# Kernel optimization log

Hardware: AMD Instinct MI355X
Metric: run time of the kernel (lower is better)

Reference implementation:

```python
import jax, jax.numpy as jnp
import numpy as np

G = 7  # grid size hardcoded in the original loops


def _xyxy(t, off, m, n):
    # t: (B, C, G, G); channels off..off+3 are (x_off, y_off, w, h)
    cx = (t[:, off + 0] + m) / G
    cy = (t[:, off + 1] + n) / G
    w = t[:, off + 2]
    h = t[:, off + 3]
    return cx - w / 2, cy - h / 2, cx + w / 2, cy + h / 2


def _iou(a, b):
    ix1 = jnp.maximum(a[0], b[0])
    iy1 = jnp.maximum(a[1], b[1])
    ix2 = jnp.minimum(a[2], b[2])
    iy2 = jnp.minimum(a[3], b[3])
    inter = jnp.maximum(ix2 - ix1, 0.0) * jnp.maximum(iy2 - iy1, 0.0)
    area_a = (a[2] - a[0]) * (a[3] - a[1])
    area_b = (b[2] - b[0]) * (b[3] - b[1])
    return jnp.where(inter > 0, inter / (area_a + area_b - inter), 0.0)


def setup_inputs() -> dict:
    key = jax.random.key(0)
    k1, k2, k3 = jax.random.split(key, 3)
    B = 8192
    pred = jax.random.uniform(k1, (B, 30, G, G), dtype=jnp.float32)
    labels = jax.random.uniform(k2, (B, 30, G, G), dtype=jnp.float32)
    # objectness channel must be exactly 1.0 for cells containing objects
    obj = (jax.random.uniform(k3, (B, G, G)) < 0.3).astype(jnp.float32)
    labels = labels.at[:, 4].set(obj)
    return {"pred": pred, "labels": labels}


def reference(pred, labels):
    B = pred.shape[0]
    dt = pred.dtype
    m = jnp.arange(G, dtype=dt)[:, None]  # index along dim -2 (as in loop var m)
    n = jnp.arange(G, dtype=dt)[None, :]  # index along dim -1 (loop var n)

    b1 = _xyxy(pred, 0, m, n)
    b2 = _xyxy(pred, 5, m, n)
    gt = _xyxy(labels, 0, m, n)
    iou1 = _iou(b1, gt)  # (B, G, G)
    iou2 = _iou(b2, gt)
    use1 = iou1 >= iou2
    obj = labels[:, 4] == 1.0

    coor1 = (jnp.sum((pred[:, 0:2] - labels[:, 0:2]) ** 2, axis=1)
             + jnp.sum((jnp.sqrt(pred[:, 2:4]) - jnp.sqrt(labels[:, 2:4])) ** 2, axis=1))
    coor2 = (jnp.sum((pred[:, 5:7] - labels[:, 5:7]) ** 2, axis=1)
             + jnp.sum((jnp.sqrt(pred[:, 7:9]) - jnp.sqrt(labels[:, 7:9])) ** 2, axis=1))
    coor = 5.0 * jnp.where(use1, coor1, coor2)

    e1 = (pred[:, 4] - iou1) ** 2
    e2 = (pred[:, 9] - iou2) ** 2
    obj_conf = jnp.where(use1, e1, e2)
    noobj_conf_objcell = 0.5 * jnp.where(use1, e2, e1)
    noobj_conf_nocell = 0.5 * (pred[:, 4] ** 2 + pred[:, 9] ** 2)

    cls = jnp.sum((pred[:, 10:] - labels[:, 10:]) ** 2, axis=1)

    per_cell = jnp.where(obj,
                         coor + obj_conf + noobj_conf_objcell + cls,
                         noobj_conf_nocell)
    return jnp.sum(per_cell) / B
```

## Files before the change

kernel.cpp:

```cpp
#include <hip/hip_runtime.h>

#define GDIM 7
#define CELLS 49
#define CH 30
#define FPB (CH * CELLS)
#define BLK 256

__device__ __forceinline__ float iou_fn(float ax1, float ay1, float ax2, float ay2,
                                        float bx1, float by1, float bx2, float by2) {
    float ix1 = fmaxf(ax1, bx1);
    float iy1 = fmaxf(ay1, by1);
    float ix2 = fminf(ax2, bx2);
    float iy2 = fminf(ay2, by2);
    float iw = fmaxf(ix2 - ix1, 0.0f);
    float ih = fmaxf(iy2 - iy1, 0.0f);
    float inter = iw * ih;
    float aa = (ax2 - ax1) * (ay2 - ay1);
    float ab = (bx2 - bx1) * (by2 - by1);
    return inter > 0.0f ? inter / (aa + ab - inter) : 0.0f;
}

__global__ __launch_bounds__(BLK) void yolo_stage1(const float* __restrict__ pred,
                                                   const float* __restrict__ lab,
                                                   float* __restrict__ partial) {
    const int tid = threadIdx.x;
    const int i = blockIdx.x * BLK + tid;

    const int b = i / CELLS;
    const int cell = i - b * CELLS;
    const int mr = cell / GDIM;
    const int nc = cell - mr * GDIM;
    const float* p = pred + (size_t)b * FPB + cell;
    const float* l = lab  + (size_t)b * FPB + cell;

    float pv[10], lv[10];
    #pragma unroll
    for (int c = 0; c < 10; ++c) pv[c] = p[c * CELLS];
    #pragma unroll
    for (int c = 0; c < 10; ++c) lv[c] = l[c * CELLS];

    float cls = 0.0f;
    #pragma unroll
    for (int c = 10; c < CH; ++c) {
        float d = p[c * CELLS] - l[c * CELLS];
        cls = fmaf(d, d, cls);
    }

    const float fm = (float)mr, fn = (float)nc;

    float gcx = (lv[0] + fm) / 7.0f;
    float gcy = (lv[1] + fn) / 7.0f;
    float gx1 = gcx - lv[2] * 0.5f, gy1 = gcy - lv[3] * 0.5f;
    float gx2 = gcx + lv[2] * 0.5f, gy2 = gcy + lv[3] * 0.5f;

    float c1x = (pv[0] + fm) / 7.0f;
    float c1y = (pv[1] + fn) / 7.0f;
    float b1x1 = c1x - pv[2] * 0.5f, b1y1 = c1y - pv[3] * 0.5f;
    float b1x2 = c1x + pv[2] * 0.5f, b1y2 = c1y + pv[3] * 0.5f;

    float c2x = (pv[5] + fm) / 7.0f;
    float c2y = (pv[6] + fn) / 7.0f;
    float b2x1 = c2x - pv[7] * 0.5f, b2y1 = c2y - pv[8] * 0.5f;
    float b2x2 = c2x + pv[7] * 0.5f, b2y2 = c2y + pv[8] * 0.5f;

    float iou1 = iou_fn(b1x1, b1y1, b1x2, b1y2, gx1, gy1, gx2, gy2);
    float iou2 = iou_fn(b2x1, b2y1, b2x2, b2y2, gx1, gy1, gx2, gy2);
    bool use1 = iou1 >= iou2;

    float d0 = pv[0] - lv[0], d1 = pv[1] - lv[1];
    float s2 = sqrtf(pv[2]) - sqrtf(lv[2]);
    float s3 = sqrtf(pv[3]) - sqrtf(lv[3]);
    float coor1 = d0 * d0 + d1 * d1 + s2 * s2 + s3 * s3;

    float d5 = pv[5] - lv[5], d6 = pv[6] - lv[6];
    float s7 = sqrtf(pv[7]) - sqrtf(lv[7]);
    float s8 = sqrtf(pv[8]) - sqrtf(lv[8]);
    float coor2 = d5 * d5 + d6 * d6 + s7 * s7 + s8 * s8;

    float coor = 5.0f * (use1 ? coor1 : coor2);

    float e1 = pv[4] - iou1; e1 *= e1;
    float e2 = pv[9] - iou2; e2 *= e2;
    float obj_conf   = use1 ? e1 : e2;
    float noobj_obj  = 0.5f * (use1 ? e2 : e1);
    float noobj_none = 0.5f * (pv[4] * pv[4] + pv[9] * pv[9]);

    bool obj = (lv[4] == 1.0f);
    float per_cell = obj ? (coor + obj_conf + noobj_obj + cls) : noobj_none;

    float v = per_cell;
    #pragma unroll
    for (int off = 32; off > 0; off >>= 1) v += __shfl_down(v, off, 64);

    __shared__ float swave[BLK / 64];
    const int lane = tid & 63;
    const int wid = tid >> 6;
    if (lane == 0) swave[wid] = v;
    __syncthreads();
    if (tid == 0) {
        float s = 0.0f;
        #pragma unroll
        for (int w = 0; w < BLK / 64; ++w) s += swave[w];
        partial[blockIdx.x] = s;
    }
}

__global__ __launch_bounds__(64) void yolo_stage2(const float* __restrict__ partial,
                                                  int n, float inv_b,
                                                  float* __restrict__ out) {
    float v = 0.0f;
    for (int i = threadIdx.x; i < n; i += 64) v += partial[i];
    #pragma unroll
    for (int off = 32; off > 0; off >>= 1) v += __shfl_down(v, off, 64);
    if (threadIdx.x == 0) out[0] = v * inv_b;
}

extern "C" void kernel_launch(void* const* d_in, const int* in_sizes, int n_in,
                              void* d_out, int out_size, void* d_ws, size_t ws_size,
                              hipStream_t stream) {
    const float* pred = (const float*)d_in[0];
    const float* lab  = (const float*)d_in[1];
    int B = in_sizes[0] / FPB;
    int total_cells = B * CELLS;
    int nblocks = total_cells / BLK;

    float* partial = (float*)d_ws;
    float* out = (float*)d_out;

    yolo_stage1<<<nblocks, BLK, 0, stream>>>(pred, lab, partial);
    yolo_stage2<<<1, 64, 0, stream>>>(partial, nblocks, 1.0f / (float)B, out);
}
```

Baseline: 28.15 us.

## Stage two batches per block in LDS via float4 coalesced loads

Each block now cooperatively loads two full batch images of pred and labels with vectorized float4 global reads into shared memory. Per-cell threads then read their 30 channels from LDS instead of issuing strided scalar global loads. The final reduction kernel is widened to 256 threads with a cross-wave shared-memory sum. The aim is better memory efficiency on this bandwidth-bound kernel. The cost is about 23.5 KB of LDS per block, which caps occupancy, and only 98 of 256 threads doing the compute.

```diff
diff --git a/kernel.cpp b/kernel.cpp
--- a/kernel.cpp
+++ b/kernel.cpp
@@ -4,7 +4,9 @@
 #define CELLS 49
 #define CH 30
 #define FPB (CH * CELLS)
+#define BPB 2
 #define BLK 256
+#define NF4 ((BPB * FPB) / 4)
 
 __device__ __forceinline__ float iou_fn(float ax1, float ay1, float ax2, float ay2,
                                         float bx1, float by1, float bx2, float by2) {
@@ -23,76 +25,101 @@
 __global__ __launch_bounds__(BLK) void yolo_stage1(const float* __restrict__ pred,
                                                    const float* __restrict__ lab,
                                                    float* __restrict__ partial) {
+    __shared__ float4 sp4[NF4];
+    __shared__ float4 sl4[NF4];
+    __shared__ float swave[BLK / 64];
+
     const int tid = threadIdx.x;
-    const int i = blockIdx.x * BLK + tid;
 
-    const int b = i / CELLS;
-    const int cell = i - b * CELLS;
-    const int mr = cell / GDIM;
-    const int nc = cell - mr * GDIM;
-    const float* p = pred + (size_t)b * FPB + cell;
-    const float* l = lab  + (size_t)b * FPB + cell;
+    const size_t base_f = (size_t)blockIdx.x * (BPB * FPB);
+    const float4* pg = (const float4*)(pred + base_f);
+    const float4* lg = (const float4*)(lab + base_f);
 
-    float pv[10], lv[10];
-    #pragma unroll
-    for (int c = 0; c < 10; ++c) pv[c] = p[c * CELLS];
-    #pragma unroll
-    for (int c = 0; c < 10; ++c) lv[c] = l[c * CELLS];
+    float4 a0 = pg[tid];
+    float4 c0 = lg[tid];
+    float4 a1 = pg[tid + 256];
+    float4 c1 = lg[tid + 256];
+    float4 a2, c2;
+    const bool t3 = tid < (NF4 - 512);
+    if (t3) { a2 = pg[tid + 512]; c2 = lg[tid + 512]; }
 
-    float cls = 0.0f;
-    #pragma unroll
-    for (int c = 10; c < CH; ++c) {
-        float d = p[c * CELLS] - l[c * CELLS];
-        cls = fmaf(d, d, cls);
+    sp4[tid] = a0;        sl4[tid] = c0;
+    sp4[tid + 256] = a1;  sl4[tid + 256] = c1;
+    if (t3) { sp4[tid + 512] = a2; sl4[tid + 512] = c2; }
+    __syncthreads();
+
+    const float* spf = (const float*)sp4;
+    const float* slf = (const float*)sl4;
+
+    float per_cell = 0.0f;
+    if (tid < BPB * CELLS) {
+        const int bl = tid / CELLS;
+        const int cell = tid - bl * CELLS;
+        const int mr = cell / GDIM;
+        const int nc = cell - mr * GDIM;
+        const float* p = spf + bl * FPB + cell;
+        const float* l = slf + bl * FPB + cell;
+
+        float pv[10], lv[10];
+        #pragma unroll
+        for (int c = 0; c < 10; ++c) pv[c] = p[c * CELLS];
+        #pragma unroll
+        for (int c = 0; c < 10; ++c) lv[c] = l[c * CELLS];
+
+        float cls = 0.0f;
+        #pragma unroll
+        for (int c = 10; c < CH; ++c) {
+            float d = p[c * CELLS] - l[c * CELLS];
+            cls = fmaf(d, d, cls);
+        }
+
+        const float fm = (float)mr, fn = (float)nc;
+
+        float gcx = (lv[0] + fm) / 7.0f;
+        float gcy = (lv[1] + fn) / 7.0f;
+        float gx1 = gcx - lv[2] * 0.5f, gy1 = gcy - lv[3] * 0.5f;
+        float gx2 = gcx + lv[2] * 0.5f, gy2 = gcy + lv[3] * 0.5f;
+
+        float c1x = (pv[0] + fm) / 7.0f;
+        float c1y = (pv[1] + fn) / 7.0f;
+        float b1x1 = c1x - pv[2] * 0.5f, b1y1 = c1y - pv[3] * 0.5f;
+        float b1x2 = c1x + pv[2] * 0.5f, b1y2 = c1y + pv[3] * 0.5f;
+
+        float c2x = (pv[5] + fm) / 7.0f;
+        float c2y = (pv[6] + fn) / 7.0f;
+        float b2x1 = c2x - pv[7] * 0.5f, b2y1 = c2y - pv[8] * 0.5f;
+        float b2x2 = c2x + pv[7] * 0.5f, b2y2 = c2y + pv[8] * 0.5f;
+
+        float iou1 = iou_fn(b1x1, b1y1, b1x2, b1y2, gx1, gy1, gx2, gy2);
+        float iou2 = iou_fn(b2x1, b2y1, b2x2, b2y2, gx1, gy1, gx2, gy2);
+        bool use1 = iou1 >= iou2;
+
+        float d0 = pv[0] - lv[0], d1 = pv[1] - lv[1];
+        float s2 = sqrtf(pv[2]) - sqrtf(lv[2]);
+        float s3 = sqrtf(pv[3]) - sqrtf(lv[3]);
+        float coor1 = d0 * d0 + d1 * d1 + s2 * s2 + s3 * s3;
+
+        float d5 = pv[5] - lv[5], d6 = pv[6] - lv[6];
+        float s7 = sqrtf(pv[7]) - sqrtf(lv[7]);
+        float s8 = sqrtf(pv[8]) - sqrtf(lv[8]);
+        float coor2 = d5 * d5 + d6 * d6 + s7 * s7 + s8 * s8;
+
+        float coor = 5.0f * (use1 ? coor1 : coor2);
+
+        float e1 = pv[4] - iou1; e1 *= e1;
+        float e2 = pv[9] - iou2; e2 *= e2;
+        float obj_conf   = use1 ? e1 : e2;
+        float noobj_obj  = 0.5f * (use1 ? e2 : e1);
+        float noobj_none = 0.5f * (pv[4] * pv[4] + pv[9] * pv[9]);
+
+        bool obj = (lv[4] == 1.0f);
+        per_cell = obj ? (coor + obj_conf + noobj_obj + cls) : noobj_none;
     }
-
-    const float fm = (float)mr, fn = (float)nc;
-
-    float gcx = (lv[0] + fm) / 7.0f;
-    float gcy = (lv[1] + fn) / 7.0f;
-    float gx1 = gcx - lv[2] * 0.5f, gy1 = gcy - lv[3] * 0.5f;
-    float gx2 = gcx + lv[2] * 0.5f, gy2 = gcy + lv[3] * 0.5f;
-
-    float c1x = (pv[0] + fm) / 7.0f;
-    float c1y = (pv[1] + fn) / 7.0f;
-    float b1x1 = c1x - pv[2] * 0.5f, b1y1 = c1y - pv[3] * 0.5f;
-    float b1x2 = c1x + pv[2] * 0.5f, b1y2 = c1y + pv[3] * 0.5f;
-
-    float c2x = (pv[5] + fm) / 7.0f;
-    float c2y = (pv[6] + fn) / 7.0f;
-    float b2x1 = c2x - pv[7] * 0.5f, b2y1 = c2y - pv[8] * 0.5f;
-    float b2x2 = c2x + pv[7] * 0.5f, b2y2 = c2y + pv[8] * 0.5f;
-
-    float iou1 = iou_fn(b1x1, b1y1, b1x2, b1y2, gx1, gy1, gx2, gy2);
-    float iou2 = iou_fn(b2x1, b2y1, b2x2, b2y2, gx1, gy1, gx2, gy2);
-    bool use1 = iou1 >= iou2;
-
-    float d0 = pv[0] - lv[0], d1 = pv[1] - lv[1];
-    float s2 = sqrtf(pv[2]) - sqrtf(lv[2]);
-    float s3 = sqrtf(pv[3]) - sqrtf(lv[3]);
-    float coor1 = d0 * d0 + d1 * d1 + s2 * s2 + s3 * s3;
-
-    float d5 = pv[5] - lv[5], d6 = pv[6] - lv[6];
-    float s7 = sqrtf(pv[7]) - sqrtf(lv[7]);
-    float s8 = sqrtf(pv[8]) - sqrtf(lv[8]);
-    float coor2 = d5 * d5 + d6 * d6 + s7 * s7 + s8 * s8;
-
-    float coor = 5.0f * (use1 ? coor1 : coor2);
-
-    float e1 = pv[4] - iou1; e1 *= e1;
-    float e2 = pv[9] - iou2; e2 *= e2;
-    float obj_conf   = use1 ? e1 : e2;
-    float noobj_obj  = 0.5f * (use1 ? e2 : e1);
-    float noobj_none = 0.5f * (pv[4] * pv[4] + pv[9] * pv[9]);
-
-    bool obj = (lv[4] == 1.0f);
-    float per_cell = obj ? (coor + obj_conf + noobj_obj + cls) : noobj_none;
 
     float v = per_cell;
     #pragma unroll
     for (int off = 32; off > 0; off >>= 1) v += __shfl_down(v, off, 64);
 
-    __shared__ float swave[BLK / 64];
     const int lane = tid & 63;
     const int wid = tid >> 6;
     if (lane == 0) swave[wid] = v;
@@ -105,14 +132,25 @@
     }
 }
 
-__global__ __launch_bounds__(64) void yolo_stage2(const float* __restrict__ partial,
-                                                  int n, float inv_b,
-                                                  float* __restrict__ out) {
+__global__ __launch_bounds__(BLK) void yolo_stage2(const float* __restrict__ partial,
+                                                   int n, float inv_b,
+                                                   float* __restrict__ out) {
     float v = 0.0f;
-    for (int i = threadIdx.x; i < n; i += 64) v += partial[i];
+    for (int i = threadIdx.x; i < n; i += BLK) v += partial[i];
     #pragma unroll
     for (int off = 32; off > 0; off >>= 1) v += __shfl_down(v, off, 64);
-    if (threadIdx.x == 0) out[0] = v * inv_b;
+
+    __shared__ float sdata[BLK / 64];
+    int lane = threadIdx.x & 63;
+    int wid  = threadIdx.x >> 6;
+    if (lane == 0) sdata[wid] = v;
+    __syncthreads();
+    if (threadIdx.x == 0) {
+        float s = 0.0f;
+        #pragma unroll
+        for (int w = 0; w < BLK / 64; ++w) s += sdata[w];
+        out[0] = s * inv_b;
+    }
 }
 
 extern "C" void kernel_launch(void* const* d_in, const int* in_sizes, int n_in,
@@ -121,12 +159,11 @@
     const float* pred = (const float*)d_in[0];
     const float* lab  = (const float*)d_in[1];
     int B = in_sizes[0] / FPB;
-    int total_cells = B * CELLS;
-    int nblocks = total_cells / BLK;
+    int nblocks = B / BPB;
 
     float* partial = (float*)d_ws;
     float* out = (float*)d_out;
 
     yolo_stage1<<<nblocks, BLK, 0, stream>>>(pred, lab, partial);
-    yolo_stage2<<<1, 64, 0, stream>>>(partial, nblocks, 1.0f / (float)B, out);
+    yolo_stage2<<<1, BLK, 0, stream>>>(partial, nblocks, 1.0f / (float)B, out);
 }
```

Result: faster. 26.16 us (-7.1%).
